# Optimization experiments

Hardware: AMD Instinct MI355X
Metric: run time of the kernel (lower is better)

Reference implementation:

```python
import jax, jax.numpy as jnp
import numpy as np

# dataset config constants
FOV_UP = 3.0 / 180.0 * np.pi
FOV_DOWN = -25.0 / 180.0 * np.pi
FOV_RANGE = abs(FOV_DOWN) + abs(FOV_UP)
DEPTH_SCALE = 6.0
DEPTH_MIN, DEPTH_MAX = 1.0, 63.0
LOG_SCALE = True
H, W = 64, 2048
B = 64


def _trig_buffers():
    scan_x = np.arange(W, dtype=np.float64) / W          # (W,)
    scan_y = np.arange(H, dtype=np.float64) / H          # (H,)
    yaw = np.pi * (scan_x * 2.0 - 1.0)                   # (W,)
    pitch = (1.0 - scan_y) * FOV_RANGE - abs(FOV_DOWN)   # (H,)
    yaw2d = np.broadcast_to(yaw[None, :], (H, W))
    pitch2d = np.broadcast_to(pitch[:, None], (H, W))
    f32 = lambda a: jnp.asarray(a, dtype=jnp.float32)
    return (f32(np.cos(yaw2d)), f32(np.sin(yaw2d)),
            f32(np.cos(pitch2d)), f32(np.sin(pitch2d)))


def setup_inputs() -> dict:
    key = jax.random.key(0)
    x = jax.random.normal(key, (B, 1, H, W), dtype=jnp.float32)
    return {"x": x}


def _range2xyz(imgs):
    cos_yaw, sin_yaw, cos_pitch, sin_pitch = _trig_buffers()
    depth = (imgs * 0.5 + 0.5) * DEPTH_SCALE              # (B,1,H,W)
    if LOG_SCALE:
        depth = jnp.exp2(depth) - 1.0
    depth = jnp.clip(depth, DEPTH_MIN, DEPTH_MAX)
    bx = cos_yaw * cos_pitch * depth
    by = -sin_yaw * cos_pitch * depth
    bz = sin_pitch * depth
    return jnp.concatenate([bx, by, bz], axis=1)          # (B,3,H,W)


def _curvature(xyz):
    # 1x11 depthwise conv along W, kernel [1]*5 + [-10] + [1]*5, pad 5
    k = jnp.array([1, 1, 1, 1, 1, -10, 1, 1, 1, 1, 1], dtype=jnp.float32)
    rhs = jnp.tile(k.reshape(1, 1, 1, 11), (3, 1, 1, 1))  # (O=3, I/g=1, 1, 11)
    d = jax.lax.conv_general_dilated(
        xyz, rhs, window_strides=(1, 1), padding=[(0, 0), (5, 5)],
        dimension_numbers=("NCHW", "OIHW", "NCHW"), feature_group_count=3)
    cloud_curvature = jnp.sum(d * d, axis=1, keepdims=True)   # (B,1,H,W)

    depth = jnp.sqrt(jnp.sum(xyz * xyz, axis=1))              # (B,H,W)
    dxyz = xyz[:, :, :, 1:] - xyz[:, :, :, :-1]               # (B,3,H,W-1)
    diff = jnp.sqrt(jnp.sum(dxyz * dxyz, axis=1))             # (B,H,W-1)
    zpad = jnp.zeros((B, H, 1), dtype=xyz.dtype)
    diff = jnp.concatenate([diff, zpad], axis=-1)             # (B,H,W)
    mask1 = diff > 0.1

    depth_ratio = depth[:, :, 1:] / depth[:, :, :-1]          # (B,H,W-1)
    dr = xyz[:, :, :, 1:] - xyz[:, :, :, :-1] * depth_ratio[:, None]
    diff_ratio = jnp.sqrt(jnp.sum(dr * dr, axis=1))           # (B,H,W-1)
    opad = jnp.ones((B, H, 1), dtype=xyz.dtype)
    diff_ratio = jnp.concatenate([opad, diff_ratio], axis=-1)
    mask2 = diff_ratio < 0.1

    picked = jnp.zeros((B, H, W), dtype=bool)
    picked = picked.at[:, :, 5:-6].set(mask1[:, :, 5:-6] & mask2[:, :, 5:-6])

    # diff2 in the original is mathematically identical to diff (squared diffs)
    diff2 = diff
    dis = jnp.sum(xyz * xyz, axis=1)                          # (B,H,W)
    outlier = (diff > 0.0002 * dis) & (diff2 > 0.0002 * dis)
    picked = picked | outlier

    inf = jnp.asarray(jnp.inf, dtype=cloud_curvature.dtype)
    return jnp.where(picked[:, None, :, :], inf, cloud_curvature)


def reference(x):
    x = x / 2.0 + 0.5
    xyz = _range2xyz(x)
    return _curvature(xyz)
```

## Files before the change

### kernel.cpp

```cpp
#include <hip/hip_runtime.h>
#include <math.h>

#define WW 2048
#define HH 64
#define NROW 4096

#define PICKED_F_BITS 0x7F7F0000u

typedef float f32x4 __attribute__((ext_vector_type(4)));
typedef float f32x2 __attribute__((ext_vector_type(2)));
typedef unsigned int u32x4 __attribute__((ext_vector_type(4)));

static __device__ inline int adr(int sc) { return sc + (sc >> 3); }

__global__ __launch_bounds__(256, 4) void curv_kernel(
    const float* __restrict__ x, unsigned short* __restrict__ out) {
  __shared__ float sd[2324];

  const int t   = threadIdx.x;
  const int row = blockIdx.x;
  const int h   = row & (HH - 1);
  const size_t base = (size_t)row * WW;
  const int c0  = 8 * t;

  f32x4 x0 = *(const f32x4*)(x + base + c0);
  f32x4 x1 = *(const f32x4*)(x + base + c0 + 4);

  if (t < 8) sd[adr(t)] = 0.0f;
  else if (t >= 248) sd[adr(t + 1808)] = 0.0f;

  const float inv2pi = 0.15915494309189535f;
  const float prad =
      (1.0f - (float)h * (1.0f / 64.0f)) * 0.48869219055841229f
      - 0.43633231299858238f;
  const float cp  = __builtin_amdgcn_cosf(prad * inv2pi);
  const float sp  = __builtin_amdgcn_sinf(prad * inv2pi);
  const float sp2 = sp * sp;
  const float cp2 = cp * cp;

  const float C1    = 4.706190423e-6f;
  const float gamma = 2.0f - 2.0f * C1 * cp2;
  const float Q     = 1062.4329f * __builtin_amdgcn_rcpf(cp2);

  const float CDU[18] = {
      0.99988234745421256f, 0.99992470183914450f, 0.99995764455196390f,
      0.99998117528260111f, 0.99999529380957619f, 1.0f,
      0.99999529380957619f, 0.99998117528260111f, 0.99995764455196390f,
      0.99992470183914450f, 0.99988234745421256f, 0.99983058179582340f,
      0.99976940535121528f, 0.99969881869620425f, 0.99961882249517864f,
      0.99952941750109314f, 0.99943060455546173f, 0.99932238458834954f};
  const float SDU[18] = {
      -0.015339206284988102f, -0.012271538285719925f, -0.0092037547820598194f,
      -0.0061358846491544753f, -0.0030679567629659763f, 0.0f,
      0.0030679567629659763f, 0.0061358846491544753f, 0.0092037547820598194f,
      0.012271538285719925f, 0.015339206284988102f, 0.018406729905804820f,
      0.021474080275469508f, 0.024541228522912288f, 0.027608145778965740f,
      0.030674803176636626f, 0.033741171851377587f, 0.036807222941358832f};

  float wd[18];

  #pragma unroll
  for (int e = 0; e < 8; ++e) {
    const float v = (e < 4) ? x0[e] : x1[e - 4];
    const float arg = __builtin_amdgcn_fmed3f(v * 1.5f + 4.5f, 1.0f, 6.0f);
    const float dpt = __builtin_amdgcn_exp2f(arg) - 1.0f;
    wd[5 + e] = dpt;
    sd[adr(c0 + 8 + e)] = dpt;
  }
  __syncthreads();

  #pragma unroll
  for (int i = 0; i < 5; ++i) {
    wd[i]      = sd[adr(c0 + 3 + i)];
    wd[13 + i] = sd[adr(c0 + 16 + i)];
  }

  f32x2 SXY = {0.f, 0.f};
  float Sw = 0.f;
  #pragma unroll
  for (int u = 0; u <= 10; ++u) {
    const f32x2 cdu = {CDU[u], SDU[u]};
    SXY = SXY + wd[u] * cdu;
    Sw += wd[u];
  }

  const bool tn0 = (t != 0), tn255 = (t != 255);
  const float pickedf = __builtin_bit_cast(float, PICKED_F_BITS);
  u32x4 ov;

  #pragma unroll
  for (int p = 0; p < 4; ++p) {
    const int j0 = 2 * p, j1 = 2 * p + 1;
    if (p > 0) {
      const float eW = wd[j0 + 10], lW = wd[j0 - 1];
      const f32x2 cE = {CDU[j0 + 10], SDU[j0 + 10]};
      const f32x2 cL = {-CDU[j0 - 1], -SDU[j0 - 1]};
      SXY = SXY + eW * cE + lW * cL;
      Sw += eW - lW;
    }
    const f32x2 S0 = SXY;
    const float S0w = Sw;
    {
      const float eW = wd[j1 + 10], lW = wd[j1 - 1];
      const f32x2 cE = {CDU[j1 + 10], SDU[j1 + 10]};
      const f32x2 cL = {-CDU[j1 - 1], -SDU[j1 - 1]};
      SXY = SXY + eW * cE + lW * cL;
      Sw += eW - lW;
    }

    const float cd0 = wd[j0 + 5], cd1 = wd[j1 + 5];
    const float nd0 = wd[j0 + 6], nd1 = wd[j1 + 6];

    const f32x2 cc0 = {-11.0f * CDU[j0 + 5], -11.0f * SDU[j0 + 5]};
    const f32x2 cc1 = {-11.0f * CDU[j1 + 5], -11.0f * SDU[j1 + 5]};
    const f32x2 dxy0 = S0 + cd0 * cc0;
    const f32x2 dxy1 = SXY + cd1 * cc1;
    const f32x2 q0 = dxy0 * dxy0, q1 = dxy1 * dxy1;

    const f32x2 cdp = {cd0, cd1}, ndp = {nd0, nd1};
    const f32x2 tdz = cdp * -11.0f + f32x2{S0w, Sw};
    const f32x2 xy2 = {q0.x + q0.y, q1.x + q1.y};
    const f32x2 curv = xy2 * cp2 + (tdz * tdz) * sp2;

    const f32x2 dis_c = cdp * cdp;
    const f32x2 dis_n = ndp * ndp;
    const f32x2 m     = cdp * ndp;
    f32x2 d2 = (dis_c + dis_n) - m * gamma;
    if (p == 3) d2.y = tn255 ? d2.y : 0.0f;
    const f32x2 sv = dis_c * 2.0e-4f;
    const f32x2 s2 = sv * sv;

    const bool wok0 = (j0 < 2) ? tn0 : ((j0 < 5) ? (tn0 && tn255) : tn255);
    const bool wok1 = (j1 < 2) ? tn0 : ((j1 < 5) ? (tn0 && tn255) : tn255);
    const bool p0 =
        ((d2.x > 0.01f) && (dis_c.x < Q) && wok0) || (d2.x > s2.x);
    const bool p1 =
        ((d2.y > 0.01f) && (dis_c.y < Q) && wok1) || (d2.y > s2.y);
    const float r0 = p0 ? pickedf : curv.x;
    const float r1 = p1 ? pickedf : curv.y;

    ov[p] = __builtin_amdgcn_perm(
        __builtin_bit_cast(unsigned int, r1),
        __builtin_bit_cast(unsigned int, r0), 0x07060302u);
  }
  *(u32x4*)(out + base + c0) = ov;
}

extern "C" void kernel_launch(void* const* d_in, const int* in_sizes, int n_in,
                              void* d_out, int out_size, void* d_ws, size_t ws_size,
                              hipStream_t stream) {
  const float* x = (const float*)d_in[0];
  unsigned short* out = (unsigned short*)d_out;
  (void)d_ws; (void)ws_size; (void)in_sizes; (void)n_in; (void)out_size;
  curv_kernel<<<NROW, 256, 0, stream>>>(x, out);
}
```

Baseline: 14.38 us.

## Process four rows per block with double-buffered LDS and next-row prefetch

Each block now handles four consecutive rows instead of one, so the grid shrinks to a quarter. Shared memory is double-buffered, which lets one barrier per row suffice, and the next row's global load is issued right after the barrier so it overlaps the current row's compute. This cuts block launch overhead and hides load latency, at the cost of fewer blocks (1024) on a large GPU, which may lower parallelism and occupancy.

```diff
diff --git a/kernel.cpp b/kernel.cpp
--- a/kernel.cpp
+++ b/kernel.cpp
@@ -4,6 +4,8 @@
 #define WW 2048
 #define HH 64
 #define NROW 4096
+#define RPB 4
+#define NBLK (NROW / RPB)
 
 #define PICKED_F_BITS 0x7F7F0000u
 
@@ -15,32 +17,14 @@
 
 __global__ __launch_bounds__(256, 4) void curv_kernel(
     const float* __restrict__ x, unsigned short* __restrict__ out) {
-  __shared__ float sd[2324];
+  __shared__ float sd[2 * 2324];
 
-  const int t   = threadIdx.x;
-  const int row = blockIdx.x;
-  const int h   = row & (HH - 1);
-  const size_t base = (size_t)row * WW;
-  const int c0  = 8 * t;
-
-  f32x4 x0 = *(const f32x4*)(x + base + c0);
-  f32x4 x1 = *(const f32x4*)(x + base + c0 + 4);
-
-  if (t < 8) sd[adr(t)] = 0.0f;
-  else if (t >= 248) sd[adr(t + 1808)] = 0.0f;
-
+  const int t  = threadIdx.x;
+  const int c0 = 8 * t;
+  const bool tn0 = (t != 0), tn255 = (t != 255);
+  const float pickedf = __builtin_bit_cast(float, PICKED_F_BITS);
   const float inv2pi = 0.15915494309189535f;
-  const float prad =
-      (1.0f - (float)h * (1.0f / 64.0f)) * 0.48869219055841229f
-      - 0.43633231299858238f;
-  const float cp  = __builtin_amdgcn_cosf(prad * inv2pi);
-  const float sp  = __builtin_amdgcn_sinf(prad * inv2pi);
-  const float sp2 = sp * sp;
-  const float cp2 = cp * cp;
-
-  const float C1    = 4.706190423e-6f;
-  const float gamma = 2.0f - 2.0f * C1 * cp2;
-  const float Q     = 1062.4329f * __builtin_amdgcn_rcpf(cp2);
+  const float C1 = 4.706190423e-6f;
 
   const float CDU[18] = {
       0.99988234745421256f, 0.99992470183914450f, 0.99995764455196390f,
@@ -57,93 +41,124 @@
       0.021474080275469508f, 0.024541228522912288f, 0.027608145778965740f,
       0.030674803176636626f, 0.033741171851377587f, 0.036807222941358832f};
 
-  float wd[18];
+  size_t base = (size_t)(RPB * blockIdx.x) * WW;
+  f32x4 x0 = *(const f32x4*)(x + base + c0);
+  f32x4 x1 = *(const f32x4*)(x + base + c0 + 4);
 
   #pragma unroll
-  for (int e = 0; e < 8; ++e) {
-    const float v = (e < 4) ? x0[e] : x1[e - 4];
-    const float arg = __builtin_amdgcn_fmed3f(v * 1.5f + 4.5f, 1.0f, 6.0f);
-    const float dpt = __builtin_amdgcn_exp2f(arg) - 1.0f;
-    wd[5 + e] = dpt;
-    sd[adr(c0 + 8 + e)] = dpt;
-  }
-  __syncthreads();
+  for (int it = 0; it < RPB; ++it) {
+    const int row = RPB * blockIdx.x + it;
+    const int h   = row & (HH - 1);
+    float* sb = sd + (it & 1) * 2324;
 
-  #pragma unroll
-  for (int i = 0; i < 5; ++i) {
-    wd[i]      = sd[adr(c0 + 3 + i)];
-    wd[13 + i] = sd[adr(c0 + 16 + i)];
-  }
+    const float prad =
+        (1.0f - (float)h * (1.0f / 64.0f)) * 0.48869219055841229f
+        - 0.43633231299858238f;
+    const float cp  = __builtin_amdgcn_cosf(prad * inv2pi);
+    const float sp  = __builtin_amdgcn_sinf(prad * inv2pi);
+    const float sp2 = sp * sp;
+    const float cp2 = cp * cp;
+    const float gamma = 2.0f - 2.0f * C1 * cp2;
+    const float Q = 1062.4329f * __builtin_amdgcn_rcpf(cp2);
 
-  f32x2 SXY = {0.f, 0.f};
-  float Sw = 0.f;
-  #pragma unroll
-  for (int u = 0; u <= 10; ++u) {
-    const f32x2 cdu = {CDU[u], SDU[u]};
-    SXY = SXY + wd[u] * cdu;
-    Sw += wd[u];
-  }
+    if (t < 8) sb[adr(t)] = 0.0f;
+    else if (t >= 248) sb[adr(t + 1808)] = 0.0f;
 
-  const bool tn0 = (t != 0), tn255 = (t != 255);
-  const float pickedf = __builtin_bit_cast(float, PICKED_F_BITS);
-  u32x4 ov;
+    float wd[18];
 
-  #pragma unroll
-  for (int p = 0; p < 4; ++p) {
-    const int j0 = 2 * p, j1 = 2 * p + 1;
-    if (p > 0) {
-      const float eW = wd[j0 + 10], lW = wd[j0 - 1];
-      const f32x2 cE = {CDU[j0 + 10], SDU[j0 + 10]};
-      const f32x2 cL = {-CDU[j0 - 1], -SDU[j0 - 1]};
-      SXY = SXY + eW * cE + lW * cL;
-      Sw += eW - lW;
+    #pragma unroll
+    for (int e = 0; e < 8; ++e) {
+      const float v = (e < 4) ? x0[e] : x1[e - 4];
+      const float arg = __builtin_amdgcn_fmed3f(v * 1.5f + 4.5f, 1.0f, 6.0f);
+      const float dpt = __builtin_amdgcn_exp2f(arg) - 1.0f;
+      wd[5 + e] = dpt;
+      sb[adr(c0 + 8 + e)] = dpt;
     }
-    const f32x2 S0 = SXY;
-    const float S0w = Sw;
-    {
-      const float eW = wd[j1 + 10], lW = wd[j1 - 1];
-      const f32x2 cE = {CDU[j1 + 10], SDU[j1 + 10]};
-      const f32x2 cL = {-CDU[j1 - 1], -SDU[j1 - 1]};
-      SXY = SXY + eW * cE + lW * cL;
-      Sw += eW - lW;
+    __syncthreads();
+
+    f32x4 x0n = x0, x1n = x1;
+    if (it < RPB - 1) {
+      x0n = *(const f32x4*)(x + base + WW + c0);
+      x1n = *(const f32x4*)(x + base + WW + c0 + 4);
     }
 
-    const float cd0 = wd[j0 + 5], cd1 = wd[j1 + 5];
-    const float nd0 = wd[j0 + 6], nd1 = wd[j1 + 6];
+    #pragma unroll
+    for (int i = 0; i < 5; ++i) {
+      wd[i]      = sb[adr(c0 + 3 + i)];
+      wd[13 + i] = sb[adr(c0 + 16 + i)];
+    }
 
-    const f32x2 cc0 = {-11.0f * CDU[j0 + 5], -11.0f * SDU[j0 + 5]};
-    const f32x2 cc1 = {-11.0f * CDU[j1 + 5], -11.0f * SDU[j1 + 5]};
-    const f32x2 dxy0 = S0 + cd0 * cc0;
-    const f32x2 dxy1 = SXY + cd1 * cc1;
-    const f32x2 q0 = dxy0 * dxy0, q1 = dxy1 * dxy1;
+    f32x2 SXY = {0.f, 0.f};
+    float Sw = 0.f;
+    #pragma unroll
+    for (int u = 0; u <= 10; ++u) {
+      const f32x2 cdu = {CDU[u], SDU[u]};
+      SXY = SXY + wd[u] * cdu;
+      Sw += wd[u];
+    }
 
-    const f32x2 cdp = {cd0, cd1}, ndp = {nd0, nd1};
-    const f32x2 tdz = cdp * -11.0f + f32x2{S0w, Sw};
-    const f32x2 xy2 = {q0.x + q0.y, q1.x + q1.y};
-    const f32x2 curv = xy2 * cp2 + (tdz * tdz) * sp2;
+    u32x4 ov;
+    #pragma unroll
+    for (int p = 0; p < 4; ++p) {
+      const int j0 = 2 * p, j1 = 2 * p + 1;
+      if (p > 0) {
+        const float eW = wd[j0 + 10], lW = wd[j0 - 1];
+        const f32x2 cE = {CDU[j0 + 10], SDU[j0 + 10]};
+        const f32x2 cL = {-CDU[j0 - 1], -SDU[j0 - 1]};
+        SXY = SXY + eW * cE + lW * cL;
+        Sw += eW - lW;
+      }
+      const f32x2 S0 = SXY;
+      const float S0w = Sw;
+      {
+        const float eW = wd[j1 + 10], lW = wd[j1 - 1];
+        const f32x2 cE = {CDU[j1 + 10], SDU[j1 + 10]};
+        const f32x2 cL = {-CDU[j1 - 1], -SDU[j1 - 1]};
+        SXY = SXY + eW * cE + lW * cL;
+        Sw += eW - lW;
+      }
 
-    const f32x2 dis_c = cdp * cdp;
-    const f32x2 dis_n = ndp * ndp;
-    const f32x2 m     = cdp * ndp;
-    f32x2 d2 = (dis_c + dis_n) - m * gamma;
-    if (p == 3) d2.y = tn255 ? d2.y : 0.0f;
-    const f32x2 sv = dis_c * 2.0e-4f;
-    const f32x2 s2 = sv * sv;
+      const float cd0 = wd[j0 + 5], cd1 = wd[j1 + 5];
+      const float nd0 = wd[j0 + 6], nd1 = wd[j1 + 6];
 
-    const bool wok0 = (j0 < 2) ? tn0 : ((j0 < 5) ? (tn0 && tn255) : tn255);
-    const bool wok1 = (j1 < 2) ? tn0 : ((j1 < 5) ? (tn0 && tn255) : tn255);
-    const bool p0 =
-        ((d2.x > 0.01f) && (dis_c.x < Q) && wok0) || (d2.x > s2.x);
-    const bool p1 =
-        ((d2.y > 0.01f) && (dis_c.y < Q) && wok1) || (d2.y > s2.y);
-    const float r0 = p0 ? pickedf : curv.x;
-    const float r1 = p1 ? pickedf : curv.y;
+      const f32x2 cc0 = {-11.0f * CDU[j0 + 5], -11.0f * SDU[j0 + 5]};
+      const f32x2 cc1 = {-11.0f * CDU[j1 + 5], -11.0f * SDU[j1 + 5]};
+      const f32x2 dxy0 = S0 + cd0 * cc0;
+      const f32x2 dxy1 = SXY + cd1 * cc1;
+      const f32x2 q0 = dxy0 * dxy0, q1 = dxy1 * dxy1;
 
-    ov[p] = __builtin_amdgcn_perm(
-        __builtin_bit_cast(unsigned int, r1),
-        __builtin_bit_cast(unsigned int, r0), 0x07060302u);
+      const f32x2 cdp = {cd0, cd1}, ndp = {nd0, nd1};
+      const f32x2 tdz = cdp * -11.0f + f32x2{S0w, Sw};
+      const f32x2 xy2 = {q0.x + q0.y, q1.x + q1.y};
+      const f32x2 curv = xy2 * cp2 + (tdz * tdz) * sp2;
+
+      const f32x2 dis_c = cdp * cdp;
+      const f32x2 dis_n = ndp * ndp;
+      const f32x2 m     = cdp * ndp;
+      f32x2 d2 = (dis_c + dis_n) - m * gamma;
+      if (p == 3) d2.y = tn255 ? d2.y : 0.0f;
+      const f32x2 sv = dis_c * 2.0e-4f;
+      const f32x2 s2 = sv * sv;
+
+      const bool wok0 = (j0 < 2) ? tn0 : ((j0 < 5) ? (tn0 && tn255) : tn255);
+      const bool wok1 = (j1 < 2) ? tn0 : ((j1 < 5) ? (tn0 && tn255) : tn255);
+      const bool p0 =
+          ((d2.x > 0.01f) && (dis_c.x < Q) && wok0) || (d2.x > s2.x);
+      const bool p1 =
+          ((d2.y > 0.01f) && (dis_c.y < Q) && wok1) || (d2.y > s2.y);
+      const float r0 = p0 ? pickedf : curv.x;
+      const float r1 = p1 ? pickedf : curv.y;
+
+      ov[p] = __builtin_amdgcn_perm(
+          __builtin_bit_cast(unsigned int, r1),
+          __builtin_bit_cast(unsigned int, r0), 0x07060302u);
+    }
+    *(u32x4*)(out + base + c0) = ov;
+
+    base += WW;
+    x0 = x0n;
+    x1 = x1n;
   }
-  *(u32x4*)(out + base + c0) = ov;
 }
 
 extern "C" void kernel_launch(void* const* d_in, const int* in_sizes, int n_in,
@@ -152,5 +167,5 @@
   const float* x = (const float*)d_in[0];
   unsigned short* out = (unsigned short*)d_out;
   (void)d_ws; (void)ws_size; (void)in_sizes; (void)n_in; (void)out_size;
-  curv_kernel<<<NROW, 256, 0, stream>>>(x, out);
+  curv_kernel<<<NBLK, 256, 0, stream>>>(x, out);
 }
```

Result: slower. 15.49 us (+7.8%).
